# Performance work log

Hardware: AMD Instinct MI355X
Metric: run time of the kernel (lower is better)

Reference implementation:

```python
import jax, jax.numpy as jnp
import numpy as np

B = 64; SEQ = 512; PRED = 96; D = 321; HID = 2048
WIN = 64; STRIDE = WIN // 2; FT = WIN // 2 + 1
LOW = int(FT * 0.3); MID = int(FT * 0.4); HIGH = FT - LOW - MID  # 9, 13, 11
NW = SEQ // STRIDE + 1; EMBED = NW * WIN  # 17, 1088
EPS = 1e-5; SCALE = 0.02
LH = int(LOW * 2.0); MH = int(MID * 2.0); HH = int(HIGH * 2.0)  # 18, 26, 22


def _clayer(key, fan_in, fan_out):
    k1, k2, k3, k4 = jax.random.split(key, 4)
    return (jax.random.normal(k1, (fan_in, fan_out), jnp.float32) * SCALE,
            jax.random.normal(k2, (fan_in, fan_out), jnp.float32) * SCALE,
            jax.random.normal(k3, (fan_out,), jnp.float32) * SCALE,
            jax.random.normal(k4, (fan_out,), jnp.float32) * SCALE)


def setup_inputs() -> dict:
    key = jax.random.key(0)
    ks = jax.random.split(key, 12)
    inp = {}
    inp["x"] = jax.random.normal(ks[0], (B, SEQ, D), jnp.float32)
    inp["x_mark_enc"] = jax.random.normal(ks[1], (B, SEQ, 4), jnp.float32)
    inp["x_dec"] = jax.random.normal(ks[2], (B, PRED, D), jnp.float32)
    inp["x_mark_dec"] = jax.random.normal(ks[3], (B, PRED, 4), jnp.float32)
    n = jnp.arange(WIN, dtype=jnp.float32)
    inp["window"] = 0.5 * (1.0 - jnp.cos(2.0 * jnp.pi * n / WIN))  # torch.hann_window (periodic)
    inp["revin_w"] = jnp.ones((D,), jnp.float32)
    inp["revin_b"] = jnp.zeros((D,), jnp.float32)
    # low band filter: 3 complex layers LOW->LH->LH->LOW
    for i, (fi, fo) in enumerate([(LOW, LH), (LH, LH), (LH, LOW)]):
        wr, wi, br, bi = _clayer(jax.random.fold_in(ks[4], i), fi, fo)
        inp[f"low{i}_wr"], inp[f"low{i}_wi"], inp[f"low{i}_br"], inp[f"low{i}_bi"] = wr, wi, br, bi
    # mid band filter: 2 complex layers MID->MH->MID
    for i, (fi, fo) in enumerate([(MID, MH), (MH, MID)]):
        wr, wi, br, bi = _clayer(jax.random.fold_in(ks[5], i), fi, fo)
        inp[f"mid{i}_wr"], inp[f"mid{i}_wi"], inp[f"mid{i}_br"], inp[f"mid{i}_bi"] = wr, wi, br, bi
    # high band filter: 1 complex layer HIGH->HIGH
    wr, wi, br, bi = _clayer(ks[6], HIGH, HIGH)
    inp["high0_wr"], inp["high0_wi"], inp["high0_br"], inp["high0_bi"] = wr, wi, br, bi
    inp["fc1_w"] = jax.random.normal(ks[7], (EMBED, HID), jnp.float32) * SCALE
    inp["fc1_b"] = jnp.zeros((HID,), jnp.float32)
    inp["fc2_w"] = jax.random.normal(ks[8], (HID, PRED), jnp.float32) * SCALE
    inp["fc2_b"] = jnp.zeros((PRED,), jnp.float32)
    return inp


def _clin(z, wr, wi, br, bi):
    return z @ (wr + 1j * wi) + (br + 1j * bi)


def _cact(z):
    return jax.nn.leaky_relu(z.real) + 1j * jax.nn.leaky_relu(z.imag)


def reference(x, x_mark_enc, x_dec, x_mark_dec, window, revin_w, revin_b,
              low0_wr, low0_wi, low0_br, low0_bi,
              low1_wr, low1_wi, low1_br, low1_bi,
              low2_wr, low2_wi, low2_br, low2_bi,
              mid0_wr, mid0_wi, mid0_br, mid0_bi,
              mid1_wr, mid1_wi, mid1_br, mid1_bi,
              high0_wr, high0_wi, high0_br, high0_bi,
              fc1_w, fc1_b, fc2_w, fc2_b):
    # RevIN norm over time dim
    mean = jnp.mean(x, axis=1, keepdims=True)
    std = jnp.sqrt(jnp.var(x, axis=1, keepdims=True) + EPS)
    xn = (x - mean) / std * revin_w + revin_b
    xc = jnp.transpose(xn, (0, 2, 1))                      # [B, D, L]
    xp = jnp.pad(xc, ((0, 0), (0, 0), (STRIDE, STRIDE)))
    # batched window extraction (replaces python loop over windows)
    idx = jnp.arange(NW)[:, None] * STRIDE + jnp.arange(WIN)[None, :]
    seg = xp[:, :, idx]
    w = window / jnp.linalg.norm(window)
    xf = jnp.fft.rfft(seg * w, axis=-1)                    # [B, D, NW, FT] complex
    low = xf[..., :LOW]
    mid = xf[..., LOW:LOW + MID]
    high = xf[..., LOW + MID:]
    low = _clin(_cact(_clin(_cact(_clin(low, low0_wr, low0_wi, low0_br, low0_bi)),
                            low1_wr, low1_wi, low1_br, low1_bi)),
                low2_wr, low2_wi, low2_br, low2_bi)
    mid = _clin(_cact(_clin(mid, mid0_wr, mid0_wi, mid0_br, mid0_bi)),
                mid1_wr, mid1_wi, mid1_br, mid1_bi)
    high = _clin(high, high0_wr, high0_wi, high0_br, high0_bi)
    xfil = jnp.concatenate([low, mid, high], axis=-1)      # [B, D, NW, FT]
    xt = jnp.fft.irfft(xfil, n=WIN, axis=-1)
    emb = xt.reshape(x.shape[0], D, EMBED)
    h = jax.nn.leaky_relu(emb @ fc1_w + fc1_b)
    y = h @ fc2_w + fc2_b                                  # [B, D, PRED]
    y = jnp.transpose(y, (0, 2, 1))                        # [B, PRED, D]
    # RevIN denorm
    y = (y - revin_b) / (revin_w + EPS * EPS) * std + mean
    return y
```

## Files before the change

### kernel.cpp

```cpp
#include <hip/hip_runtime.h>

typedef unsigned short u16;
typedef unsigned int   u32;
typedef __attribute__((ext_vector_type(4))) float  fvec4;
typedef __attribute__((ext_vector_type(8))) __bf16 bvec8;

#define NB    64
#define SEQL  512
#define DCH   321
#define BDTOT (NB * DCH)
#define NWIN  17
#define PREDL 96
#define MWTOT (BDTOT * NWIN)
#define KPAD  1152

__device__ __forceinline__ u16 f2bf(float f) {
    union { float f; u32 u; } v; v.f = f;
    u32 r = v.u + 0x7FFFu + ((v.u >> 16) & 1u);
    return (u16)(r >> 16);
}
__device__ __forceinline__ float lrelu(float v) { return v > 0.f ? v : 0.01f * v; }

__device__ __forceinline__ void gld16(const u16* g, u16* l) {
    __builtin_amdgcn_global_load_lds((const __attribute__((address_space(1))) void*)g,
                                     (__attribute__((address_space(3))) void*)l, 16, 0, 0);
}

__global__ __launch_bounds__(256) void stats_kernel(const float* __restrict__ x,
                                                    float* __restrict__ mean,
                                                    float* __restrict__ rstd,
                                                    float* __restrict__ stdv) {
    __shared__ float ls[2][4][64];
    int i = threadIdx.x & 63;
    int j = threadIdx.x >> 6;
    int bd = blockIdx.x * 64 + i;
    int b = bd / DCH, d = bd - b * DCH;
    float s = 0.f, ss = 0.f;
    for (int t = j; t < SEQL; t += 4) {
        float v = x[((size_t)b * SEQL + t) * DCH + d];
        s += v; ss += v * v;
    }
    ls[0][j][i] = s; ls[1][j][i] = ss;
    __syncthreads();
    if (j == 0) {
        s  = ls[0][0][i] + ls[0][1][i] + ls[0][2][i] + ls[0][3][i];
        ss = ls[1][0][i] + ls[1][1][i] + ls[1][2][i] + ls[1][3][i];
        float m   = s * (1.f / SEQL);
        float var = ss * (1.f / SEQL) - m * m;
        float st  = sqrtf(var + 1e-5f);
        mean[bd] = m; rstd[bd] = 1.f / st; stdv[bd] = st;
    }
}

__global__ __launch_bounds__(256) void norm_transpose(const float* __restrict__ x,
                                                      const float* __restrict__ mean,
                                                      const float* __restrict__ rstd,
                                                      const float* __restrict__ rw,
                                                      const float* __restrict__ rb,
                                                      u16* __restrict__ xnT) {
    __shared__ float tile[64][65];
    int d0 = blockIdx.x * 64, s0 = blockIdx.y * 64, b = blockIdx.z;
    for (int e = threadIdx.x; e < 4096; e += 256) {
        int sr = e >> 6, dc = e & 63;
        int d = d0 + dc;
        tile[sr][dc] = (d < DCH) ? x[((size_t)b * SEQL + s0 + sr) * DCH + d] : 0.f;
    }
    __syncthreads();
    for (int e = threadIdx.x; e < 4096; e += 256) {
        int dr = e >> 6, sc = e & 63;
        int d = d0 + dr;
        if (d < DCH) {
            int bd = b * DCH + d;
            float v = (tile[sc][dr] - mean[bd]) * rstd[bd] * rw[d] + rb[d];
            xnT[(size_t)bd * 576 + 32 + s0 + sc] = f2bf(v);
        }
    }
}

__global__ __launch_bounds__(256) void pads(u16* __restrict__ xnT, u16* __restrict__ EMB) {
    int idx = blockIdx.x * 256 + threadIdx.x;
    if (idx < BDTOT * 64) {
        int bd = idx >> 6, q = idx & 63;
        int off = q < 32 ? q : 512 + q;
        xnT[(size_t)bd * 576 + off] = 0;
    } else if (idx < BDTOT * 64 + BDTOT * 8) {
        int t = idx - BDTOT * 64;
        int bd = t >> 3, o = (t & 7) * 8;
        fvec4 z = {0.f, 0.f, 0.f, 0.f};
        *(fvec4*)&EMB[(size_t)bd * KPAD + 1088 + o] = z;
    }
}

__global__ __launch_bounds__(256) void precompute_kernel(
    const float* __restrict__ window,
    const float* __restrict__ l0wr, const float* __restrict__ l0wi,
    const float* __restrict__ l0br, const float* __restrict__ l0bi,
    const float* __restrict__ l1wr, const float* __restrict__ l1wi,
    const float* __restrict__ l1br, const float* __restrict__ l1bi,
    const float* __restrict__ l2wr, const float* __restrict__ l2wi,
    const float* __restrict__ l2br, const float* __restrict__ l2bi,
    const float* __restrict__ m0wr, const float* __restrict__ m0wi,
    const float* __restrict__ m0br, const float* __restrict__ m0bi,
    const float* __restrict__ m1wr, const float* __restrict__ m1wi,
    const float* __restrict__ m1br, const float* __restrict__ m1bi,
    const float* __restrict__ h0wr, const float* __restrict__ h0wi,
    const float* __restrict__ h0br, const float* __restrict__ h0bi,
    u16* __restrict__ A1t, u16* __restrict__ W1t, u16* __restrict__ B2t,
    float* __restrict__ bias1, float* __restrict__ bias2, float* __restrict__ biast)
{
    int idx = blockIdx.x * 256 + threadIdx.x;
    float nrm = 0.f;
    for (int i = 0; i < 64; ++i) nrm += window[i] * window[i];
    float inv = 1.0f / sqrtf(nrm);
    const float STEP = 6.283185307179586f / 64.f;
    auto Cc = [&](int n, int k) { return  window[n] * inv * cosf(STEP * (float)((k * n) & 63)); };
    auto Ss = [&](int n, int k) { return -window[n] * inv * sinf(STEP * (float)((k * n) & 63)); };
    auto aRe = [&](int k, int n) {
        float sc = (k == 0 || k == 32) ? (1.f / 64.f) : (2.f / 64.f);
        return sc * cosf(STEP * (float)((k * n) & 63));
    };
    auto aIm = [&](int k, int n) {
        if (k == 0 || k == 32) return 0.f;
        return -(2.f / 64.f) * sinf(STEP * (float)((k * n) & 63));
    };
    if (idx < 16384) {
        int j = idx >> 6, n = idx & 63;
        float v = 0.f;
        if (j < 18)                    { for (int k = 0; k < 9;  ++k) v += Cc(n,k)   *l0wr[k*18+j]      - Ss(n,k)   *l0wi[k*18+j]; }
        else if (j < 36)               { int jj=j-18; for (int k = 0; k < 9;  ++k) v += Cc(n,k)   *l0wi[k*18+jj] + Ss(n,k)   *l0wr[k*18+jj]; }
        else if (j >= 64  && j < 90)   { int jj=j-64; for (int k = 0; k < 13; ++k) v += Cc(n,9+k) *m0wr[k*26+jj] - Ss(n,9+k) *m0wi[k*26+jj]; }
        else if (j >= 90  && j < 116)  { int jj=j-90; for (int k = 0; k < 13; ++k) v += Cc(n,9+k) *m0wi[k*26+jj] + Ss(n,9+k) *m0wr[k*26+jj]; }
        else if (j >= 128 && j < 139)  { int jj=j-128;for (int k = 0; k < 11; ++k) v += Cc(n,22+k)*h0wr[k*11+jj] - Ss(n,22+k)*h0wi[k*11+jj]; }
        else if (j >= 139 && j < 150)  { int jj=j-139;for (int k = 0; k < 11; ++k) v += Cc(n,22+k)*h0wi[k*11+jj] + Ss(n,22+k)*h0wr[k*11+jj]; }
        A1t[idx] = f2bf(v);
    } else if (idx < 24576) {
        int t = idx - 16384; int j = t >> 6, k = t & 63;
        float v = 0.f;
        if (j < 18)      { if (k < 18) v = l1wr[k*18+j];        else if (k < 36) v = -l1wi[(k-18)*18+j]; }
        else if (j < 36) { int jj=j-18; if (k < 18) v = l1wi[k*18+jj]; else if (k < 36) v =  l1wr[(k-18)*18+jj]; }
        W1t[t] = f2bf(v);
    } else if (idx < 49152) {
        int t = idx - 24576; int n = t / 192, c = t - n * 192;
        float v = 0.f;
        if (n < 64) {
            if (c < 18)                  { for (int m = 0; m < 9;  ++m) v +=  l2wr[c*9+m]     *aRe(m,n)   + l2wi[c*9+m]     *aIm(m,n); }
            else if (c < 36)             { int cc=c-18; for (int m = 0; m < 9;  ++m) v += -l2wi[cc*9+m]   *aRe(m,n)   + l2wr[cc*9+m]   *aIm(m,n); }
            else if (c >= 64 && c < 90)  { int cc=c-64; for (int m = 0; m < 13; ++m) v +=  m1wr[cc*13+m]  *aRe(9+m,n) + m1wi[cc*13+m]  *aIm(9+m,n); }
            else if (c >= 90 && c < 116) { int cc=c-90; for (int m = 0; m < 13; ++m) v += -m1wi[cc*13+m]  *aRe(9+m,n) + m1wr[cc*13+m]  *aIm(9+m,n); }
            else if (c >= 128 && c < 139){ v = aRe(22 + (c-128), n); }
            else if (c >= 139 && c < 150){ v = aIm(22 + (c-139), n); }
        }
        B2t[t] = f2bf(v);
    } else if (idx < 49344) {
        int c = idx - 49152;
        float v = 0.f;
        if (c < 18) v = l0br[c];
        else if (c < 36) v = l0bi[c-18];
        else if (c >= 64 && c < 90) v = m0br[c-64];
        else if (c >= 90 && c < 116) v = m0bi[c-90];
        bias1[c] = v;
    } else if (idx < 49472) {
        int c = idx - 49344;
        float v = 0.f;
        if (c < 18) v = l1br[c]; else if (c < 36) v = l1bi[c-18];
        bias2[c] = v;
    } else if (idx < 49536) {
        int n = idx - 49472;
        float v = 0.f;
        for (int k = 0; k <= 32; ++k) {
            float br = (k < 9) ? l2br[k] : (k < 22 ? m1br[k-9] : h0br[k-22]);
            float bi = (k < 9) ? l2bi[k] : (k < 22 ? m1bi[k-9] : h0bi[k-22]);
            v += aRe(k, n) * br + aIm(k, n) * bi;
        }
        biast[n] = v;
    }
}

__global__ __launch_bounds__(256) void wtrans(const float* __restrict__ W, u16* __restrict__ Wt,
                                              int R, int C, int Cpad, int ldw) {
    __shared__ float t[32][33];
    int c0 = blockIdx.x * 32, r0 = blockIdx.y * 32;
    for (int e = threadIdx.x; e < 1024; e += 256) {
        int rr = e >> 5, cc = e & 31;
        int rg = r0 + rr, cg = c0 + cc;
        t[rr][cc] = (rg < R && cg < C) ? W[(size_t)rg * C + cg] : 0.f;
    }
    __syncthreads();
    for (int e = threadIdx.x; e < 1024; e += 256) {
        int cr = e >> 5, rc = e & 31;
        int cg = c0 + cr, rg = r0 + rc;
        if (cg < Cpad && rg < ldw) Wt[(size_t)cg * ldw + rg] = f2bf(t[rc][cr]);
    }
}

__global__ __launch_bounds__(256) void spectral_fused(
    const u16* __restrict__ xnT, const u16* __restrict__ A1t,
    const u16* __restrict__ W1t, const u16* __restrict__ B2t,
    const float* __restrict__ bias1, const float* __restrict__ bias2,
    const float* __restrict__ biast, u16* __restrict__ EMB)
{
    __shared__ u16 XB[64 * 72];
    __shared__ u16 ACT[64 * 208];
    const int tid  = threadIdx.x;
    const int lane = tid & 63;
    const int wn   = tid >> 6;
    const int r0   = blockIdx.x * 64;

    {
        int rr = tid >> 2;
        int cc = (tid & 3) * 16;
        u32 gr = (u32)(r0 + rr);
        u32 bd = gr / 17u, nw = gr - bd * 17u;
        const u16* src = xnT + (size_t)bd * 576 + nw * 32 + cc;
        *(bvec8*)&XB[rr * 72 + cc]     = *(const bvec8*)(src);
        *(bvec8*)&XB[rr * 72 + cc + 8] = *(const bvec8*)(src + 8);
    }
    __syncthreads();

    fvec4 acc1[4][3] = {};
#pragma unroll
    for (int kk = 0; kk < 2; ++kk) {
        int ko = kk * 32 + ((lane >> 4) << 3);
        bvec8 af[4], bf[3];
#pragma unroll
        for (int m = 0; m < 4; ++m)
            af[m] = *(const bvec8*)&XB[(m * 16 + (lane & 15)) * 72 + ko];
#pragma unroll
        for (int n = 0; n < 3; ++n)
            bf[n] = *(const bvec8*)(A1t + (size_t)(wn * 48 + n * 16 + (lane & 15)) * 64 + ko);
#pragma unroll
        for (int m = 0; m < 4; ++m)
#pragma unroll
            for (int n = 0; n < 3; ++n)
                acc1[m][n] = __builtin_amdgcn_mfma_f32_16x16x32_bf16(af[m], bf[n], acc1[m][n], 0, 0, 0);
    }
#pragma unroll
    for (int n = 0; n < 3; ++n) {
        int col = wn * 48 + n * 16 + (lane & 15);
        float bs = bias1[col];
#pragma unroll
        for (int m = 0; m < 4; ++m)
#pragma unroll
            for (int q = 0; q < 4; ++q) {
                int row = m * 16 + ((lane >> 4) << 2) + q;
                float v = acc1[m][n][q] + bs;
                if (col < 128) v = lrelu(v);
                ACT[row * 208 + col] = f2bf(v);
            }
    }
    __syncthreads();

    fvec4 acc2[4] = {};
#pragma unroll
    for (int kk = 0; kk < 2; ++kk) {
        int ko = kk * 32 + ((lane >> 4) << 3);
        bvec8 bf = *(const bvec8*)(W1t + (size_t)(wn * 16 + (lane & 15)) * 64 + ko);
#pragma unroll
        for (int m = 0; m < 4; ++m) {
            bvec8 af = *(const bvec8*)&ACT[(m * 16 + (lane & 15)) * 208 + ko];
            acc2[m] = __builtin_amdgcn_mfma_f32_16x16x32_bf16(af, bf, acc2[m], 0, 0, 0);
        }
    }
    __syncthreads();
    {
        int col = wn * 16 + (lane & 15);
        float bs = bias2[col];
#pragma unroll
        for (int m = 0; m < 4; ++m)
#pragma unroll
            for (int q = 0; q < 4; ++q) {
                int row = m * 16 + ((lane >> 4) << 2) + q;
                ACT[row * 208 + col] = f2bf(lrelu(acc2[m][q] + bs));
            }
    }
    __syncthreads();

    fvec4 acc3[4] = {};
#pragma unroll
    for (int kk = 0; kk < 6; ++kk) {
        int ko = kk * 32 + ((lane >> 4) << 3);
        bvec8 bf = *(const bvec8*)(B2t + (size_t)(wn * 16 + (lane & 15)) * 192 + ko);
#pragma unroll
        for (int m = 0; m < 4; ++m) {
            bvec8 af = *(const bvec8*)&ACT[(m * 16 + (lane & 15)) * 208 + ko];
            acc3[m] = __builtin_amdgcn_mfma_f32_16x16x32_bf16(af, bf, acc3[m], 0, 0, 0);
        }
    }
    {
        int col = wn * 16 + (lane & 15);
        float bs = biast[col];
#pragma unroll
        for (int m = 0; m < 4; ++m)
#pragma unroll
            for (int q = 0; q < 4; ++q) {
                int row = m * 16 + ((lane >> 4) << 2) + q;
                int wr = r0 + row;
                int bd2 = wr / 17, nw2 = wr - bd2 * 17;
                EMB[(size_t)bd2 * KPAD + nw2 * 64 + col] = f2bf(acc3[m][q] + bs);
            }
    }
}

template <int SWZ>
__global__ __launch_bounds__(512, 2) void gemm_fused(
    const u16* __restrict__ A, const u16* __restrict__ Bt,
    const float* __restrict__ bias, const u16* __restrict__ W2t,
    float* __restrict__ YP,
    int Mloc, int K, long long a_off, int nwg)
{
    extern __shared__ u16 lds[];
    const int tid  = threadIdx.x;
    const int lane = tid & 63;
    const int l15  = lane & 15;
    const int hi   = lane >> 4;
    const int wid  = tid >> 6;
    const int wm   = wid >> 2;
    const int wn   = wid & 3;
    int wg;
    if (SWZ) {
        int bid = blockIdx.x;
        int q = nwg >> 3, r = nwg & 7, xcd = bid & 7, off = bid >> 3;
        wg = (xcd < r) ? (xcd * (q + 1) + off) : (r * (q + 1) + (xcd - r) * q + off);
    } else wg = blockIdx.x;
    const int mt = wg >> 3;
    const int nt = wg & 7;
    const int bm0 = mt * 256, bn0 = nt * 256;

    const u16* sbase[4][2];
#pragma unroll
    for (int u = 0; u < 4; ++u) {
#pragma unroll
        for (int j = 0; j < 2; ++j) {
            int idx = j * 512 + tid;
            if ((u & 1) == 0) {
                int row = (u >> 1) * 128 + (idx >> 3);
                int kc = ((idx & 7) ^ (row & 7)) << 3;
                int rl = bm0 + row; if (rl > Mloc - 1) rl = Mloc - 1;
                sbase[u][j] = A + (size_t)(a_off + rl) * K + kc;
            } else {
                int row = idx >> 2;
                int kc = (u >> 1) * 32 + (((idx & 3) ^ ((row >> 1) & 3)) << 3);
                sbase[u][j] = Bt + (size_t)(bn0 + row) * K + kc;
            }
        }
    }
    auto stage_unit = [&](int bufb, int tg, int u) {
        int base = ((u & 1) == 0) ? ((u >> 1) * 8192) : (16384 + (u >> 1) * 8192);
        u16* dstb = lds + bufb * 32768 + base;
#pragma unroll
        for (int j = 0; j < 2; ++j) {
            int idx = j * 512 + tid;
            gld16(sbase[u][j] + ((size_t)tg << 6), dstb + idx * 8);
        }
    };

    fvec4 acc[8][4] = {};
    const int NT = K >> 6;

    stage_unit(0, 0, 0); stage_unit(0, 0, 1); stage_unit(0, 0, 2); stage_unit(0, 0, 3);
    asm volatile("s_waitcnt vmcnt(4)");
    __builtin_amdgcn_s_barrier();

    for (int t = 0; t < NT; ++t) {
        const int cur = t & 1;
        const u16* Ab = lds + cur * 32768;
        const u16* Bb = Ab + 16384;
        const bool nl = (t < NT - 1);
        bvec8 bfr[4];
#pragma unroll
        for (int p = 0; p < 4; ++p) {
            const int kk = p >> 1, mh = p & 1;
            bvec8 af[4];
            if (mh == 0) {
#pragma unroll
                for (int n = 0; n < 4; ++n) {
                    int r = wn * 64 + n * 16 + l15;
                    int ch = hi ^ ((r >> 1) & 3);
                    bfr[n] = *(const bvec8*)&Bb[kk * 8192 + r * 32 + ch * 8];
                }
            }
#pragma unroll
            for (int mm = 0; mm < 4; ++mm) {
                int r = mh * 128 + wm * 64 + mm * 16 + l15;
                int ch = (kk * 4 + hi) ^ (r & 7);
                af[mm] = *(const bvec8*)&Ab[r * 64 + ch * 8];
            }
            if (nl) stage_unit(cur ^ 1, t + 1, p);
            __builtin_amdgcn_s_barrier();
            asm volatile("s_waitcnt lgkmcnt(0)");
            __builtin_amdgcn_s_setprio(1);
#pragma unroll
            for (int mm = 0; mm < 4; ++mm)
#pragma unroll
                for (int n = 0; n < 4; ++n)
                    acc[mh * 4 + mm][n] = __builtin_amdgcn_mfma_f32_16x16x32_bf16(
                        af[mm], bfr[n], acc[mh * 4 + mm][n], 0, 0, 0);
            __builtin_amdgcn_s_setprio(0);
            if (p == 0) {
                if (nl) asm volatile("s_waitcnt vmcnt(4)");
                else    asm volatile("s_waitcnt vmcnt(2)");
            } else if (p == 1) {
                if (nl) asm volatile("s_waitcnt vmcnt(4)");
                else    asm volatile("s_waitcnt vmcnt(0)");
            } else if (p == 3) {
                if (nl) asm volatile("s_waitcnt vmcnt(4)");
            }
            __builtin_amdgcn_s_barrier();
        }
    }

#pragma unroll
    for (int m = 0; m < 8; ++m) {
        int mh = m >> 2, mm = m & 3;
        int row0 = mh * 128 + wm * 64 + mm * 16 + hi * 4;
#pragma unroll
        for (int n = 0; n < 4; ++n) {
            int col = wn * 64 + n * 16 + l15;
            float bs = bias[bn0 + col];
#pragma unroll
            for (int q = 0; q < 4; ++q) {
                int r = row0 + q;
                lds[r * 256 + (((col >> 3) ^ (r & 7)) << 3) + (col & 7)] =
                    f2bf(lrelu(acc[m][n][q] + bs));
            }
        }
    }
    __syncthreads();

    fvec4 acc2[2][6] = {};
    const int wr0 = wid * 32;
#pragma unroll
    for (int ks = 0; ks < 8; ++ks) {
        bvec8 bw[6];
#pragma unroll
        for (int cf = 0; cf < 6; ++cf)
            bw[cf] = *(const bvec8*)(W2t + (size_t)(cf * 16 + l15) * 2048 + bn0 + ks * 32 + hi * 8);
#pragma unroll
        for (int rf = 0; rf < 2; ++rf) {
            int r = wr0 + rf * 16 + l15;
            bvec8 ah = *(const bvec8*)&lds[r * 256 + (((ks * 4 + hi) ^ (r & 7)) << 3)];
#pragma unroll
            for (int cf = 0; cf < 6; ++cf)
                acc2[rf][cf] = __builtin_amdgcn_mfma_f32_16x16x32_bf16(ah, bw[cf], acc2[rf][cf], 0, 0, 0);
        }
    }
    float* yp = YP + (size_t)nt * ((size_t)BDTOT * PREDL);
#pragma unroll
    for (int rf = 0; rf < 2; ++rf) {
#pragma unroll
        for (int cf = 0; cf < 6; ++cf) {
#pragma unroll
            for (int q = 0; q < 4; ++q) {
                int r = bm0 + wr0 + rf * 16 + hi * 4 + q;
                if (r < Mloc) yp[(size_t)r * PREDL + cf * 16 + l15] = acc2[rf][cf][q];
            }
        }
    }
}

__global__ __launch_bounds__(256) void final_denorm(const float* __restrict__ YP,
                                                    const float* __restrict__ fc2b,
                                                    const float* __restrict__ mean,
                                                    const float* __restrict__ stdv,
                                                    const float* __restrict__ rw,
                                                    const float* __restrict__ rb,
                                                    float* __restrict__ out) {
    const size_t PART = (size_t)BDTOT * PREDL;
    __shared__ float t[32][33];
    int d0 = blockIdx.x * 32, p0 = blockIdx.y * 32, b = blockIdx.z;
    for (int e = threadIdx.x; e < 1024; e += 256) {
        int di = e >> 5, pj = e & 31;
        int d = d0 + di, p = p0 + pj;
        if (d < DCH && p < PREDL) {
            size_t off = ((size_t)b * DCH + d) * PREDL + p;
            float s = fc2b[p];
#pragma unroll
            for (int i = 0; i < 8; ++i) s += YP[off + (size_t)i * PART];
            t[di][pj] = s;
        } else t[di][pj] = 0.f;
    }
    __syncthreads();
    for (int e = threadIdx.x; e < 1024; e += 256) {
        int pi = e >> 5, dj = e & 31;
        int d = d0 + dj, p = p0 + pi;
        if (d < DCH && p < PREDL) {
            int bd = b * DCH + d;
            float v = (t[dj][pi] - rb[d]) / (rw[d] + 1e-10f) * stdv[bd] + mean[bd];
            out[((size_t)b * PREDL + p) * DCH + d] = v;
        }
    }
}

extern "C" void kernel_launch(void* const* d_in, const int* in_sizes, int n_in,
                              void* d_out, int out_size, void* d_ws, size_t ws_size,
                              hipStream_t stream) {
    const float* x      = (const float*)d_in[0];
    const float* window = (const float*)d_in[4];
    const float* rw     = (const float*)d_in[5];
    const float* rb     = (const float*)d_in[6];
    const float* l0wr = (const float*)d_in[7],  *l0wi = (const float*)d_in[8];
    const float* l0br = (const float*)d_in[9],  *l0bi = (const float*)d_in[10];
    const float* l1wr = (const float*)d_in[11], *l1wi = (const float*)d_in[12];
    const float* l1br = (const float*)d_in[13], *l1bi = (const float*)d_in[14];
    const float* l2wr = (const float*)d_in[15], *l2wi = (const float*)d_in[16];
    const float* l2br = (const float*)d_in[17], *l2bi = (const float*)d_in[18];
    const float* m0wr = (const float*)d_in[19], *m0wi = (const float*)d_in[20];
    const float* m0br = (const float*)d_in[21], *m0bi = (const float*)d_in[22];
    const float* m1wr = (const float*)d_in[23], *m1wi = (const float*)d_in[24];
    const float* m1br = (const float*)d_in[25], *m1bi = (const float*)d_in[26];
    const float* h0wr = (const float*)d_in[27], *h0wi = (const float*)d_in[28];
    const float* h0br = (const float*)d_in[29], *h0bi = (const float*)d_in[30];
    const float* fc1w = (const float*)d_in[31];
    const float* fc1b = (const float*)d_in[32];
    const float* fc2w = (const float*)d_in[33];
    const float* fc2b = (const float*)d_in[34];

    char* p = (char*)d_ws;
    auto alloc = [&](size_t n) { char* r = p; p += (n + 255) & ~(size_t)255; return r; };
    float* mean  = (float*)alloc(BDTOT * 4);
    float* rstd  = (float*)alloc(BDTOT * 4);
    float* stdv  = (float*)alloc(BDTOT * 4);
    float* bias1 = (float*)alloc(192 * 4);
    float* bias2 = (float*)alloc(128 * 4);
    float* biast = (float*)alloc(64 * 4);
    u16* A1t   = (u16*)alloc(256 * 64 * 2);
    u16* W1t   = (u16*)alloc(128 * 64 * 2);
    u16* B2t   = (u16*)alloc(128 * 192 * 2);
    u16* fc1wT = (u16*)alloc((size_t)2048 * KPAD * 2);
    u16* fc2wT = (u16*)alloc((size_t)128 * 2048 * 2);
    u16* xnT   = (u16*)alloc((size_t)BDTOT * 576 * 2);
    u16* EMB   = (u16*)alloc((size_t)BDTOT * KPAD * 2);
    float* YP  = (float*)alloc((size_t)8 * BDTOT * PREDL * 4);

    hipFuncSetAttribute(reinterpret_cast<const void*>(&gemm_fused<1>),
                        hipFuncAttributeMaxDynamicSharedMemorySize, 131072);

    dim3 blk(256);
    stats_kernel<<<BDTOT / 64, blk, 0, stream>>>(x, mean, rstd, stdv);
    norm_transpose<<<dim3(6, 8, NB), blk, 0, stream>>>(x, mean, rstd, rw, rb, xnT);
    pads<<<(BDTOT * 72 + 255) / 256, blk, 0, stream>>>(xnT, EMB);
    precompute_kernel<<<194, blk, 0, stream>>>(window,
        l0wr, l0wi, l0br, l0bi, l1wr, l1wi, l1br, l1bi, l2wr, l2wi, l2br, l2bi,
        m0wr, m0wi, m0br, m0bi, m1wr, m1wi, m1br, m1bi, h0wr, h0wi, h0br, h0bi,
        A1t, W1t, B2t, bias1, bias2, biast);
    wtrans<<<dim3(64, 36), blk, 0, stream>>>(fc1w, fc1wT, 1088, 2048, 2048, KPAD);
    wtrans<<<dim3(4, 64),  blk, 0, stream>>>(fc2w, fc2wT, 2048, 96, 128, 2048);

    spectral_fused<<<MWTOT / 64, blk, 0, stream>>>(xnT, A1t, W1t, B2t, bias1, bias2, biast, EMB);

    {
        int gm = (BDTOT + 255) / 256;
        int nwg = 8 * gm;
        gemm_fused<1><<<dim3(nwg), dim3(512), 131072, stream>>>(EMB, fc1wT, fc1b, fc2wT, YP,
            BDTOT, KPAD, 0, nwg);
    }
    final_denorm<<<dim3(11, 3, NB), blk, 0, stream>>>(YP, fc2b, mean, stdv, rw, rb, (float*)d_out);
}
```

Before: 295.3 us.

## Simplify GEMM main loop to whole-tile prefetch with single barrier per step

Replaces the four-phase interleaved staging in the fc1 GEMM main loop (per-quarter async loads, explicit vmcnt waits and two barriers per phase) with a single prefetch of the whole next k-tile at the start of each iteration followed by all MFMAs and one __syncthreads. This cuts barrier count and waitcnt bookkeeping but relies on the compiler-inserted full waits, which may reduce overlap of global loads with compute. Separately, the spectral kernel's activation LDS row pitch changes from 208 to 200 elements to alter bank mapping.

Measured after the change: 293.5 us. Within noise of the previous version (-0.6%).

```diff
diff --git a/kernel.cpp b/kernel.cpp
--- a/kernel.cpp
+++ b/kernel.cpp
@@ -200,7 +200,7 @@
     const float* __restrict__ biast, u16* __restrict__ EMB)
 {
     __shared__ u16 XB[64 * 72];
-    __shared__ u16 ACT[64 * 208];
+    __shared__ u16 ACT[64 * 200];
     const int tid  = threadIdx.x;
     const int lane = tid & 63;
     const int wn   = tid >> 6;
@@ -245,7 +245,7 @@
                 int row = m * 16 + ((lane >> 4) << 2) + q;
                 float v = acc1[m][n][q] + bs;
                 if (col < 128) v = lrelu(v);
-                ACT[row * 208 + col] = f2bf(v);
+                ACT[row * 200 + col] = f2bf(v);
             }
     }
     __syncthreads();
@@ -257,7 +257,7 @@
         bvec8 bf = *(const bvec8*)(W1t + (size_t)(wn * 16 + (lane & 15)) * 64 + ko);
 #pragma unroll
         for (int m = 0; m < 4; ++m) {
-            bvec8 af = *(const bvec8*)&ACT[(m * 16 + (lane & 15)) * 208 + ko];
+            bvec8 af = *(const bvec8*)&ACT[(m * 16 + (lane & 15)) * 200 + ko];
             acc2[m] = __builtin_amdgcn_mfma_f32_16x16x32_bf16(af, bf, acc2[m], 0, 0, 0);
         }
     }
@@ -270,7 +270,7 @@
 #pragma unroll
             for (int q = 0; q < 4; ++q) {
                 int row = m * 16 + ((lane >> 4) << 2) + q;
-                ACT[row * 208 + col] = f2bf(lrelu(acc2[m][q] + bs));
+                ACT[row * 200 + col] = f2bf(lrelu(acc2[m][q] + bs));
             }
     }
     __syncthreads();
@@ -282,7 +282,7 @@
         bvec8 bf = *(const bvec8*)(B2t + (size_t)(wn * 16 + (lane & 15)) * 192 + ko);
 #pragma unroll
         for (int m = 0; m < 4; ++m) {
-            bvec8 af = *(const bvec8*)&ACT[(m * 16 + (lane & 15)) * 208 + ko];
+            bvec8 af = *(const bvec8*)&ACT[(m * 16 + (lane & 15)) * 200 + ko];
             acc3[m] = __builtin_amdgcn_mfma_f32_16x16x32_bf16(af, bf, acc3[m], 0, 0, 0);
         }
     }
@@ -326,93 +326,79 @@
     const int nt = wg & 7;
     const int bm0 = mt * 256, bn0 = nt * 256;
 
-    const u16* sbase[4][2];
-#pragma unroll
-    for (int u = 0; u < 4; ++u) {
+    const u16* sA[4];
+    const u16* sB[4];
+#pragma unroll
+    for (int j = 0; j < 4; ++j) {
+        int idx = j * 512 + tid;
+        int row = idx >> 3;
+        int kc = ((idx & 7) ^ (row & 7)) << 3;
+        int rl = bm0 + row; if (rl > Mloc - 1) rl = Mloc - 1;
+        sA[j] = A + (size_t)(a_off + rl) * K + kc;
+    }
+#pragma unroll
+    for (int kk = 0; kk < 2; ++kk)
 #pragma unroll
         for (int j = 0; j < 2; ++j) {
             int idx = j * 512 + tid;
-            if ((u & 1) == 0) {
-                int row = (u >> 1) * 128 + (idx >> 3);
-                int kc = ((idx & 7) ^ (row & 7)) << 3;
-                int rl = bm0 + row; if (rl > Mloc - 1) rl = Mloc - 1;
-                sbase[u][j] = A + (size_t)(a_off + rl) * K + kc;
-            } else {
-                int row = idx >> 2;
-                int kc = (u >> 1) * 32 + (((idx & 3) ^ ((row >> 1) & 3)) << 3);
-                sbase[u][j] = Bt + (size_t)(bn0 + row) * K + kc;
-            }
-        }
-    }
-    auto stage_unit = [&](int bufb, int tg, int u) {
-        int base = ((u & 1) == 0) ? ((u >> 1) * 8192) : (16384 + (u >> 1) * 8192);
-        u16* dstb = lds + bufb * 32768 + base;
-#pragma unroll
-        for (int j = 0; j < 2; ++j) {
-            int idx = j * 512 + tid;
-            gld16(sbase[u][j] + ((size_t)tg << 6), dstb + idx * 8);
-        }
+            int row = idx >> 2;
+            int kc = kk * 32 + (((idx & 3) ^ ((row >> 1) & 3)) << 3);
+            sB[kk * 2 + j] = Bt + (size_t)(bn0 + row) * K + kc;
+        }
+
+    auto stage_all = [&](int bufb, int tg) {
+        u16* dst = lds + bufb * 32768;
+        size_t ko = (size_t)tg << 6;
+#pragma unroll
+        for (int j = 0; j < 4; ++j)
+            gld16(sA[j] + ko, dst + (j * 512 + tid) * 8);
+#pragma unroll
+        for (int kk = 0; kk < 2; ++kk)
+#pragma unroll
+            for (int j = 0; j < 2; ++j)
+                gld16(sB[kk * 2 + j] + ko, dst + 16384 + kk * 8192 + (j * 512 + tid) * 8);
     };
 
     fvec4 acc[8][4] = {};
     const int NT = K >> 6;
 
-    stage_unit(0, 0, 0); stage_unit(0, 0, 1); stage_unit(0, 0, 2); stage_unit(0, 0, 3);
-    asm volatile("s_waitcnt vmcnt(4)");
-    __builtin_amdgcn_s_barrier();
+    stage_all(0, 0);
+    __syncthreads();
 
     for (int t = 0; t < NT; ++t) {
-        const int cur = t & 1;
-        const u16* Ab = lds + cur * 32768;
+        const u16* Ab = lds + (t & 1) * 32768;
         const u16* Bb = Ab + 16384;
-        const bool nl = (t < NT - 1);
-        bvec8 bfr[4];
-#pragma unroll
-        for (int p = 0; p < 4; ++p) {
-            const int kk = p >> 1, mh = p & 1;
-            bvec8 af[4];
-            if (mh == 0) {
-#pragma unroll
-                for (int n = 0; n < 4; ++n) {
-                    int r = wn * 64 + n * 16 + l15;
-                    int ch = hi ^ ((r >> 1) & 3);
-                    bfr[n] = *(const bvec8*)&Bb[kk * 8192 + r * 32 + ch * 8];
-                }
-            }
-#pragma unroll
-            for (int mm = 0; mm < 4; ++mm) {
-                int r = mh * 128 + wm * 64 + mm * 16 + l15;
+        if (t < NT - 1) stage_all((t + 1) & 1, t + 1);
+        __builtin_amdgcn_s_setprio(1);
+#pragma unroll
+        for (int kk = 0; kk < 2; ++kk) {
+            bvec8 bfr[4], af[8];
+#pragma unroll
+            for (int n = 0; n < 4; ++n) {
+                int r = wn * 64 + n * 16 + l15;
+                int ch = hi ^ ((r >> 1) & 3);
+                bfr[n] = *(const bvec8*)&Bb[kk * 8192 + r * 32 + ch * 8];
+            }
+#pragma unroll
+            for (int m = 0; m < 8; ++m) {
+                int r = (m >> 2) * 128 + wm * 64 + (m & 3) * 16 + l15;
                 int ch = (kk * 4 + hi) ^ (r & 7);
-                af[mm] = *(const bvec8*)&Ab[r * 64 + ch * 8];
-            }
-            if (nl) stage_unit(cur ^ 1, t + 1, p);
-            __builtin_amdgcn_s_barrier();
-            asm volatile("s_waitcnt lgkmcnt(0)");
-            __builtin_amdgcn_s_setprio(1);
-#pragma unroll
-            for (int mm = 0; mm < 4; ++mm)
+                af[m] = *(const bvec8*)&Ab[r * 64 + ch * 8];
+            }
+#pragma unroll
+            for (int m = 0; m < 8; ++m)
 #pragma unroll
                 for (int n = 0; n < 4; ++n)
-                    acc[mh * 4 + mm][n] = __builtin_amdgcn_mfma_f32_16x16x32_bf16(
-                        af[mm], bfr[n], acc[mh * 4 + mm][n], 0, 0, 0);
-            __builtin_amdgcn_s_setprio(0);
-            if (p == 0) {
-                if (nl) asm volatile("s_waitcnt vmcnt(4)");
-                else    asm volatile("s_waitcnt vmcnt(2)");
-            } else if (p == 1) {
-                if (nl) asm volatile("s_waitcnt vmcnt(4)");
-                else    asm volatile("s_waitcnt vmcnt(0)");
-            } else if (p == 3) {
-                if (nl) asm volatile("s_waitcnt vmcnt(4)");
-            }
-            __builtin_amdgcn_s_barrier();
-        }
+                    acc[m][n] = __builtin_amdgcn_mfma_f32_16x16x32_bf16(
+                        af[m], bfr[n], acc[m][n], 0, 0, 0);
+        }
+        __builtin_amdgcn_s_setprio(0);
+        __syncthreads();
     }
 
 #pragma unroll
     for (int m = 0; m < 8; ++m) {
-        int mh = m >> 2, mm = m & 3;
-        int row0 = mh * 128 + wm * 64 + mm * 16 + hi * 4;
+        int row0 = (m >> 2) * 128 + wm * 64 + (m & 3) * 16 + hi * 4;
 #pragma unroll
         for (int n = 0; n < 4; ++n) {
             int col = wn * 64 + n * 16 + l15;
```
